# Kernel optimization log

Measured on AMD Instinct MI355X. Metric: run time of the kernel, lower is better.

The kernel has to match this reference:

```python
import jax, jax.numpy as jnp
import numpy as np

B, T, E, H = 2, 4096, 1024, 16
SEGS = (256, 512, 1024, 2048, 4096)
DILS = (1, 2, 4, 8, 16)
NEG = -1e8  # torchscale uses -1e8 for uncovered / masked lse entries


def setup_inputs() -> dict:
    key = jax.random.key(0)
    ks = jax.random.split(key, 5)
    sc = 0.02
    zb = jnp.zeros((E,), jnp.float32)
    return {
        "x": jax.random.normal(ks[0], (B, T, E), jnp.float32),
        "wq": jax.random.normal(ks[1], (E, E), jnp.float32) * sc,
        "bq": zb,
        "wk": jax.random.normal(ks[2], (E, E), jnp.float32) * sc,
        "bk": zb,
        "wv": jax.random.normal(ks[3], (E, E), jnp.float32) * sc,
        "bv": zb,
        "wo": jax.random.normal(ks[4], (E, E), jnp.float32) * sc,
        "bo": zb,
    }


def _scale_attn(q, k, v, w, r):
    # One LongNet scale: segment length w, dilation ratio r.
    # Head group g = head // (H//r) attends to in-segment positions p with p % r == g
    # (torchscale dense_to_sparse diagonal over (r1, r2)).
    Bq, Tq, Hq, d = q.shape
    n, s, hp = Tq // w, w // r, Hq // r  # segments, sparse length, heads per group

    def gather(x):
        # [B,T,H,d] -> segments [B,n,w,H,d]; split w=(s,r1) (p=l*r+r1) and H=(r2,hp);
        # keep diagonal r1 == r2.
        x = x.reshape(Bq, n, s, r, r, hp, d)
        x = jnp.diagonal(x, axis1=3, axis2=4)          # [B,n,s,hp,d,r]
        return jnp.moveaxis(x, -1, 3).reshape(Bq, n, s, Hq, d)

    qs, ks_, vs = gather(q), gather(k), gather(v)
    scores = jnp.einsum('bnqhd,bnkhd->bnhqk', qs, ks_)
    mask = jnp.tril(jnp.ones((s, s), dtype=bool))       # causal within sparse segment
    scores = jnp.where(mask, scores, NEG)
    lse = jax.scipy.special.logsumexp(scores, axis=-1)  # [B,n,h,q]
    out = jnp.einsum('bnhqk,bnkhd->bnqhd', jax.nn.softmax(scores, axis=-1), vs)

    # Scatter back to dense positions (sparse_to_dense): uncovered -> out 0, lse -1e8.
    eye = jnp.eye(r, dtype=out.dtype)
    out_g = out.reshape(Bq, n, s, r, hp, d)                               # heads as (g, hp)
    dense = jnp.einsum('bnsghd,pg->bnspghd', out_g, eye).reshape(Bq, Tq, Hq, d)
    lse_g = jnp.transpose(lse, (0, 1, 3, 2)).reshape(Bq, n, s, r, hp)     # [B,n,s,g,hp]
    lse_d = jnp.where(eye[:, :, None] > 0, lse_g[:, :, :, None, :, :], NEG)
    return dense, lse_d.reshape(Bq, Tq, Hq)


def reference(x, wq, bq, wk, bk, wv, bv, wo, bo):
    d = E // H
    q = (x @ wq + bq).reshape(B, T, H, d) * (d ** -0.5)
    k = (x @ wk + bk).reshape(B, T, H, d)
    v = (x @ wv + bv).reshape(B, T, H, d)
    outs, lses = [], []
    for w_, r_ in zip(SEGS, DILS):
        o, l = _scale_attn(q, k, v, w_, r_)
        outs.append(o)
        lses.append(l)
    # Merge scales with softmax over per-scale log-sum-exp (dense-attention equivalence).
    wgt = jax.nn.softmax(jnp.stack(lses), axis=0)[..., None]  # [S,B,T,H,1]
    y = jnp.sum(jnp.stack(outs) * wgt, axis=0).reshape(B, T, E)
    return y @ wo + bo
```

## Files before the change

### kernel.cpp

```cpp
#include <hip/hip_runtime.h>
#include <hip/hip_bf16.h>

typedef __bf16 bf16_t;
typedef __bf16 bf16x8 __attribute__((ext_vector_type(8)));
typedef __bf16 bf16x4 __attribute__((ext_vector_type(4)));
typedef float f32x4 __attribute__((ext_vector_type(4)));
typedef int vint4 __attribute__((ext_vector_type(4)));

#define AS1 __attribute__((address_space(1)))
#define AS3 __attribute__((address_space(3)))

constexpr int B_ = 2, T_ = 4096, E_ = 1024, H_ = 16;
constexpr int M_ = B_ * T_;

__device__ constexpr size_t OB_OFF[5]  = {0, 8388608, 12582912, 14680064, 15728640};
__device__ constexpr size_t LSE_OFF[5] = {0, 131072, 196608, 229376, 245760};
constexpr size_t OB_TOTAL  = 16252928;
constexpr size_t LSE_TOTAL = 253952;

__global__ __launch_bounds__(256) void cvt_f32_bf16(const float* __restrict__ in,
                                                    bf16_t* __restrict__ out) {
  int i = (blockIdx.x * 256 + threadIdx.x) * 4;
  const float4 v = *(const float4*)(in + i);
  bf16x4 o;
  o[0] = (bf16_t)v.x; o[1] = (bf16_t)v.y; o[2] = (bf16_t)v.z; o[3] = (bf16_t)v.w;
  *(bf16x4*)(out + i) = o;
}

__global__ __launch_bounds__(256) void cvt_transpose_w(
    const float* __restrict__ w0, const float* __restrict__ w1,
    const float* __restrict__ w2, const float* __restrict__ w3,
    bf16_t* __restrict__ o0, bf16_t* __restrict__ o1,
    bf16_t* __restrict__ o2, bf16_t* __restrict__ o3) {
  __shared__ float tile[32][33];
  const float* src; bf16_t* dst;
  switch (blockIdx.z) {
    case 0: src = w0; dst = o0; break;
    case 1: src = w1; dst = o1; break;
    case 2: src = w2; dst = o2; break;
    default: src = w3; dst = o3; break;
  }
  const int n0 = blockIdx.x * 32, k0 = blockIdx.y * 32;
  const int tx = threadIdx.x & 31, ty = threadIdx.x >> 5;
#pragma unroll
  for (int i = 0; i < 32; i += 8)
    tile[ty + i][tx] = src[(size_t)(k0 + ty + i) * E_ + n0 + tx];
  __syncthreads();
#pragma unroll
  for (int i = 0; i < 32; i += 8)
    dst[(size_t)(n0 + ty + i) * E_ + k0 + tx] = (bf16_t)tile[tx][ty + i];
}

template <bool OUT_BF16, bool QKV>
__global__ __launch_bounds__(512, 1) void gemm256(
    const bf16_t* __restrict__ A, const bf16_t* __restrict__ BT,
    const float* __restrict__ bias0, const float* __restrict__ bias1,
    const float* __restrict__ bias2, void* __restrict__ Cout) {
  constexpr int K = E_;
  constexpr int NT = K / 64;
  __shared__ bf16_t Sm[65536];

  const int tid = threadIdx.x;
  const int lane = tid & 63;
  const int wid = tid >> 6;
  const int wm = wid >> 2, wn = wid & 3;
  const int lc = lane & 15, lg = lane >> 4;
  const int bm = blockIdx.x;
  int bn = blockIdx.y;

  const float* bias = bias0;
  float scale = 1.0f;
  void* outp = Cout;
  const bf16_t* Bt = BT;
  if (QKV) {
    const int which = bn >> 2;
    bn &= 3;
    bias = (which == 0) ? bias0 : (which == 1) ? bias1 : bias2;
    scale = (which == 0) ? 0.125f : 1.0f;
    outp = (void*)((bf16_t*)Cout + (size_t)which * M_ * E_);
    Bt += (size_t)which * E_ * E_;
  }

  const int srow = tid >> 3;
  const int schunk = (tid & 7) ^ (srow & 7);
  const bf16_t* Ag = A + (size_t)(bm * 256 + srow) * K + schunk * 8;
  const bf16_t* Bg = Bt + (size_t)(bn * 256 + srow) * K + schunk * 8;

  auto stA = [&](int kt, int bu) {
#pragma unroll
    for (int l = 0; l < 4; ++l)
      __builtin_amdgcn_global_load_lds(
          (const AS1 void*)(Ag + (size_t)(l * 64) * K + kt * 64),
          (AS3 void*)(Sm + bu * 32768 + l * 4096 + tid * 8), 16, 0, 0);
  };
  auto stB = [&](int kt, int bu) {
#pragma unroll
    for (int l = 0; l < 4; ++l)
      __builtin_amdgcn_global_load_lds(
          (const AS1 void*)(Bg + (size_t)(l * 64) * K + kt * 64),
          (AS3 void*)(Sm + bu * 32768 + 16384 + l * 4096 + tid * 8), 16, 0, 0);
  };

  f32x4 acc[8][4] = {};

  stA(0, 0); stB(0, 0);
  stA(1, 1); stB(1, 1);
  asm volatile("s_waitcnt vmcnt(8)" ::: "memory");
  __builtin_amdgcn_s_barrier();
  asm volatile("" ::: "memory");

  for (int kt = 0; kt < NT; ++kt) {
    const int bc = kt & 1;
    const bf16_t* Sa = Sm + bc * 32768;
    const bf16_t* Sb = Sm + bc * 32768 + 16384;
    const bool st = (kt + 2) < NT;

#pragma unroll
    for (int kk = 0; kk < 2; ++kk) {
      bf16x8 afr[8], bfr[4];
      const int sl = ((kk * 4 + lg) ^ (lc & 7)) * 8;
#pragma unroll
      for (int i = 0; i < 8; ++i)
        afr[i] = *(const bf16x8*)&Sa[(wm * 128 + i * 16 + lc) * 64 + sl];
#pragma unroll
      for (int j = 0; j < 4; ++j)
        bfr[j] = *(const bf16x8*)&Sb[(wn * 64 + j * 16 + lc) * 64 + sl];
      if (kk == 1 && st) {
        asm volatile("s_waitcnt lgkmcnt(0)" ::: "memory");
        __builtin_amdgcn_s_barrier();
        stA(kt + 2, bc); stB(kt + 2, bc);
      }
      __builtin_amdgcn_s_setprio(1);
#pragma unroll
      for (int i = 0; i < 8; ++i)
#pragma unroll
        for (int j = 0; j < 4; ++j)
          acc[i][j] = __builtin_amdgcn_mfma_f32_16x16x32_bf16(afr[i], bfr[j], acc[i][j], 0, 0, 0);
      __builtin_amdgcn_s_setprio(0);
    }
    if (st)                asm volatile("s_waitcnt vmcnt(8)" ::: "memory");
    else if (kt + 1 < NT)  asm volatile("s_waitcnt vmcnt(0)" ::: "memory");
    if (kt + 1 < NT) {
      __builtin_amdgcn_s_barrier();
      asm volatile("" ::: "memory");
    }
  }

#pragma unroll
  for (int i = 0; i < 8; ++i) {
    const int row = bm * 256 + wm * 128 + i * 16 + lg * 4;
#pragma unroll
    for (int j = 0; j < 4; ++j) {
      const int col = bn * 256 + wn * 64 + j * 16 + lc;
      const float bv = bias[col];
#pragma unroll
      for (int rg = 0; rg < 4; ++rg) {
        const float v = (acc[i][j][rg] + bv) * scale;
        if (OUT_BF16)
          ((bf16_t*)outp)[(size_t)(row + rg) * E_ + col] = (bf16_t)v;
        else
          ((float*)outp)[(size_t)(row + rg) * E_ + col] = v;
      }
    }
  }
}

template <bool OUT_BF16, bool QKV>
__global__ __launch_bounds__(512, 1) void gemm_dp(
    const bf16_t* __restrict__ A, const bf16_t* __restrict__ BT,
    const float* __restrict__ bias0, const float* __restrict__ bias1,
    const float* __restrict__ bias2, void* __restrict__ Cout) {
  constexpr int K = E_;
  constexpr int NT = K / 64;
  __shared__ bf16_t Sm[73728];

  const int tid = threadIdx.x;
  const int lane = tid & 63;
  const int wid = tid >> 6;
  const int wm = wid >> 1, wn = wid & 1;
  const int lc = lane & 15, lg = lane >> 4;
  const int bm = blockIdx.x;
  int bn = blockIdx.y;

  const float* bias = bias0;
  float scale = 1.0f;
  void* outp = Cout;
  const bf16_t* Bt = BT;
  if (QKV) {
    const int which = bn >> 3;
    bn &= 7;
    bias = (which == 0) ? bias0 : (which == 1) ? bias1 : bias2;
    scale = (which == 0) ? 0.125f : 1.0f;
    outp = (void*)((bf16_t*)Cout + (size_t)which * M_ * E_);
    Bt += (size_t)which * E_ * E_;
  }

  const int srow = tid >> 3;
  const int schunk = (tid & 7) ^ (srow & 7);
  const bf16_t* Ag = A + (size_t)(bm * 256 + srow) * K + schunk * 8;
  const bf16_t* Bg = Bt + (size_t)(bn * 128 + srow) * K + schunk * 8;

  auto stA = [&](int kt, int bu) {
#pragma unroll
    for (int l = 0; l < 4; ++l)
      __builtin_amdgcn_global_load_lds(
          (const AS1 void*)(Ag + (size_t)(l * 64) * K + kt * 64),
          (AS3 void*)(Sm + bu * 16384 + l * 4096 + tid * 8), 16, 0, 0);
  };
  auto stB = [&](int kt, int bu) {
#pragma unroll
    for (int l = 0; l < 2; ++l)
      __builtin_amdgcn_global_load_lds(
          (const AS1 void*)(Bg + (size_t)(l * 64) * K + kt * 64),
          (AS3 void*)(Sm + 49152 + bu * 8192 + l * 4096 + tid * 8), 16, 0, 0);
  };

  const int sl0 = ((lg) ^ (lc & 7)) * 8;
  const int sl1 = ((4 + lg) ^ (lc & 7)) * 8;

  f32x4 acc[4][4] = {};

  stA(0, 0); stB(0, 0);
  stA(1, 1); stB(1, 1);

  for (int kt = 0; kt < NT; ++kt) {
    const int bc = kt % 3;
    if (kt + 2 < NT) {
      const int bs = (kt + 2) % 3;
      stA(kt + 2, bs); stB(kt + 2, bs);
      asm volatile("s_waitcnt vmcnt(12)" ::: "memory");
    } else if (kt + 1 < NT) {
      asm volatile("s_waitcnt vmcnt(6)" ::: "memory");
    } else {
      asm volatile("s_waitcnt vmcnt(0)" ::: "memory");
    }
    __builtin_amdgcn_s_barrier();
    asm volatile("" ::: "memory");

    const int ab = bc * 16384 + (wm * 64 + lc) * 64;
    const int bb = 49152 + bc * 8192 + (wn * 64 + lc) * 64;
    bf16x8 afr[4][2], bfr[4][2];
#pragma unroll
    for (int i = 0; i < 4; ++i) {
      afr[i][0] = *(const bf16x8*)&Sm[ab + i * 1024 + sl0];
      afr[i][1] = *(const bf16x8*)&Sm[ab + i * 1024 + sl1];
    }
#pragma unroll
    for (int j = 0; j < 4; ++j) {
      bfr[j][0] = *(const bf16x8*)&Sm[bb + j * 1024 + sl0];
      bfr[j][1] = *(const bf16x8*)&Sm[bb + j * 1024 + sl1];
    }
#pragma unroll
    for (int i = 0; i < 4; ++i)
#pragma unroll
      for (int j = 0; j < 4; ++j) {
        acc[i][j] = __builtin_amdgcn_mfma_f32_16x16x32_bf16(afr[i][0], bfr[j][0], acc[i][j], 0, 0, 0);
        acc[i][j] = __builtin_amdgcn_mfma_f32_16x16x32_bf16(afr[i][1], bfr[j][1], acc[i][j], 0, 0, 0);
      }
    asm volatile("" ::: "memory");
    __builtin_amdgcn_s_barrier();
  }

#pragma unroll
  for (int i = 0; i < 4; ++i) {
    const int row = bm * 256 + wm * 64 + i * 16 + lg * 4;
#pragma unroll
    for (int j = 0; j < 4; ++j) {
      const int col = bn * 128 + wn * 64 + j * 16 + lc;
      const float bv = bias[col];
#pragma unroll
      for (int rg = 0; rg < 4; ++rg) {
        const float v = (acc[i][j][rg] + bv) * scale;
        if (OUT_BF16)
          ((bf16_t*)outp)[(size_t)(row + rg) * E_ + col] = (bf16_t)v;
        else
          ((float*)outp)[(size_t)(row + rg) * E_ + col] = v;
      }
    }
  }
}

__global__ __launch_bounds__(512, 4) void attn_inst(
    const bf16_t* __restrict__ Q, const bf16_t* __restrict__ K,
    const bf16_t* __restrict__ V, bf16_t* __restrict__ Ob,
    float* __restrict__ Lse) {
  __shared__ alignas(16) bf16_t Ks[256][72];
  __shared__ alignas(16) bf16_t Vt[64][264];
  __shared__ alignas(16) bf16_t Pw[8][16][40];

  const int bid = blockIdx.x;
  int s, ibase;
  if (bid < 512)      { s = 0; ibase = 0; }
  else if (bid < 768) { s = 1; ibase = 512; }
  else if (bid < 896) { s = 2; ibase = 768; }
  else if (bid < 960) { s = 3; ibase = 896; }
  else                { s = 4; ibase = 960; }
  const int inst = bid - ibase;
  const int h = inst & 15;
  const int nseg_log = 4 - s;
  const int seg = (inst >> 4) & ((1 << nseg_log) - 1);
  const int b = inst >> (4 + nseg_log);
  const int g = h >> (4 - s);

  const int t = threadIdx.x;
  const int lane = t & 63;
  const int wv = t >> 6;
  const int lc = lane & 15;
  const int lg = lane >> 4;

  {
    const int row = t >> 1, ch = (t & 1) * 32;
    const int tk = ((seg * 256 + row) << s) + g;
    const size_t off = ((size_t)b * T_ + tk) * E_ + h * 64 + ch;
    const bf16_t* Kg = K + off;
    const bf16_t* Vg = V + off;
#pragma unroll
    for (int j = 0; j < 4; ++j)
      *(bf16x8*)&Ks[row][ch + j * 8] = *(const bf16x8*)(Kg + j * 8);
#pragma unroll
    for (int j = 0; j < 4; ++j) {
      bf16x8 va = *(const bf16x8*)(Vg + j * 8);
#pragma unroll
      for (int e = 0; e < 8; ++e) Vt[ch + j * 8 + e][row] = va[e];
    }
  }
  __syncthreads();

  const size_t rowbase = (size_t)(b * H_ + h) * (T_ >> s) + seg * 256;

#pragma unroll
  for (int sel = 0; sel < 2; ++sel) {
    const int tile = sel ? (15 - wv) : wv;
    const int q = tile * 16 + lc;

    const int tq = ((seg * 256 + q) << s) + g;
    const bf16_t* Qg = Q + ((size_t)b * T_ + tq) * E_ + h * 64 + lg * 8;
    bf16x8 qfrag0 = *(const bf16x8*)(Qg);
    bf16x8 qfrag1 = *(const bf16x8*)(Qg + 32);

    float m = -INFINITY, Z = 0.0f;
    f32x4 Oa[4] = {};

    const int nkb = tile / 2 + 1;
    const int diag = tile / 2;
    for (int kb = 0; kb < nkb; ++kb) {
      f32x4 sacc[2] = {};
      __builtin_amdgcn_s_setprio(1);
#pragma unroll
      for (int kt = 0; kt < 2; ++kt) {
        bf16x8 kf0 = *(const bf16x8*)&Ks[kb * 32 + kt * 16 + lc][lg * 8];
        bf16x8 kf1 = *(const bf16x8*)&Ks[kb * 32 + kt * 16 + lc][32 + lg * 8];
        sacc[kt] = __builtin_amdgcn_mfma_f32_16x16x32_bf16(kf0, qfrag0, sacc[kt], 0, 0, 0);
        sacc[kt] = __builtin_amdgcn_mfma_f32_16x16x32_bf16(kf1, qfrag1, sacc[kt], 0, 0, 0);
      }
      __builtin_amdgcn_s_setprio(0);
      if (kb == diag) {
#pragma unroll
        for (int kt = 0; kt < 2; ++kt)
#pragma unroll
          for (int rg = 0; rg < 4; ++rg)
            if (kb * 32 + kt * 16 + lg * 4 + rg > q) sacc[kt][rg] = -1e30f;
      }
      float pm = fmaxf(fmaxf(fmaxf(sacc[0][0], sacc[0][1]), fmaxf(sacc[0][2], sacc[0][3])),
                       fmaxf(fmaxf(sacc[1][0], sacc[1][1]), fmaxf(sacc[1][2], sacc[1][3])));
      pm = fmaxf(pm, __shfl_xor(pm, 16));
      pm = fmaxf(pm, __shfl_xor(pm, 32));
      const float nm = fmaxf(m, pm);
      const float crr = __expf(m - nm);
      m = nm;
      float psum = 0.0f;
#pragma unroll
      for (int kt = 0; kt < 2; ++kt)
#pragma unroll
        for (int rg = 0; rg < 4; ++rg) {
          const float p = __expf(sacc[kt][rg] - nm);
          psum += p;
          Pw[wv][lc][kt * 16 + lg * 4 + rg] = (bf16_t)p;
        }
      psum += __shfl_xor(psum, 16);
      psum += __shfl_xor(psum, 32);
      Z = Z * crr + psum;
#pragma unroll
      for (int dt = 0; dt < 4; ++dt)
#pragma unroll
        for (int rg = 0; rg < 4; ++rg) Oa[dt][rg] *= crr;
      bf16x8 pb = *(const bf16x8*)&Pw[wv][lc][lg * 8];
      __builtin_amdgcn_s_setprio(1);
#pragma unroll
      for (int dt = 0; dt < 4; ++dt) {
        bf16x8 vf = *(const bf16x8*)&Vt[dt * 16 + lc][kb * 32 + lg * 8];
        Oa[dt] = __builtin_amdgcn_mfma_f32_16x16x32_bf16(vf, pb, Oa[dt], 0, 0, 0);
      }
      __builtin_amdgcn_s_setprio(0);
    }

    const float lse = m + __logf(Z);
    const float iZ = 1.0f / Z;
    bf16_t* orow = Ob + OB_OFF[s] + (rowbase + q) * 64 + lg * 4;
#pragma unroll
    for (int dt = 0; dt < 4; ++dt) {
      bf16x4 ov;
      ov[0] = (bf16_t)(Oa[dt][0] * iZ);
      ov[1] = (bf16_t)(Oa[dt][1] * iZ);
      ov[2] = (bf16_t)(Oa[dt][2] * iZ);
      ov[3] = (bf16_t)(Oa[dt][3] * iZ);
      *(bf16x4*)(orow + dt * 16) = ov;
    }
    if (lg == 0) Lse[LSE_OFF[s] + rowbase + q] = lse;
  }
}

__global__ __launch_bounds__(256) void attn_merge(const bf16_t* __restrict__ Ob,
                                                  const float* __restrict__ Lse,
                                                  bf16_t* __restrict__ Y) {
  const int gtid = blockIdx.x * 256 + threadIdx.x;
  const int d8 = gtid & 7;
  const int h = (gtid >> 3) & 15;
  const int tt = (gtid >> 7) & (T_ - 1);
  const int b = gtid >> 19;

  float m = -INFINITY, S = 0.0f;
  float acc[8];
#pragma unroll
  for (int j = 0; j < 8; ++j) acc[j] = 0.0f;

#pragma unroll
  for (int s = 0; s < 5; ++s) {
    const int r = 1 << s;
    const int g = h >> (4 - s);
    if ((tt & (r - 1)) != g) continue;
    const size_t idx = (size_t)(b * H_ + h) * (T_ >> s) + (tt >> s);
    const float lse = Lse[LSE_OFF[s] + idx];
    const bf16x8 ov = *(const bf16x8*)(Ob + OB_OFF[s] + idx * 64 + d8 * 8);
    const float nM = fmaxf(m, lse);
    const float a = __expf(m - nM);
    const float e = __expf(lse - nM);
#pragma unroll
    for (int j = 0; j < 8; ++j) acc[j] = acc[j] * a + (float)ov[j] * e;
    S = S * a + e;
    m = nM;
  }

  const float invS = 1.0f / S;
  bf16x8 o;
#pragma unroll
  for (int j = 0; j < 8; ++j) o[j] = (bf16_t)(acc[j] * invS);
  *(bf16x8*)(Y + (size_t)gtid * 8) = o;
}

extern "C" void kernel_launch(void* const* d_in, const int* in_sizes, int n_in,
                              void* d_out, int out_size, void* d_ws, size_t ws_size,
                              hipStream_t stream) {
  (void)in_sizes; (void)n_in; (void)out_size; (void)ws_size;
  const float* x  = (const float*)d_in[0];
  const float* wq = (const float*)d_in[1];
  const float* bq = (const float*)d_in[2];
  const float* wk = (const float*)d_in[3];
  const float* bk = (const float*)d_in[4];
  const float* wv = (const float*)d_in[5];
  const float* bv = (const float*)d_in[6];
  const float* wo = (const float*)d_in[7];
  const float* bo = (const float*)d_in[8];

  char* p = (char*)d_ws;
  auto take = [&](size_t bytes) {
    char* q = p;
    p += (bytes + 255) & ~(size_t)255;
    return (void*)q;
  };
  bf16_t* wq_t = (bf16_t*)take((size_t)E_ * E_ * 2);
  bf16_t* wk_t = (bf16_t*)take((size_t)E_ * E_ * 2);
  bf16_t* wv_t = (bf16_t*)take((size_t)E_ * E_ * 2);
  bf16_t* wo_t = (bf16_t*)take((size_t)E_ * E_ * 2);
  bf16_t* xb   = (bf16_t*)take((size_t)M_ * E_ * 2);
  bf16_t* qb   = (bf16_t*)take((size_t)M_ * E_ * 2);
  bf16_t* kbuf = (bf16_t*)take((size_t)M_ * E_ * 2);
  bf16_t* vbuf = (bf16_t*)take((size_t)M_ * E_ * 2);
  bf16_t* yb   = (bf16_t*)take((size_t)M_ * E_ * 2);
  bf16_t* Ob   = (bf16_t*)take(OB_TOTAL * 2);
  float*  Lse  = (float*)take(LSE_TOTAL * 4);
  (void)wk_t; (void)wv_t;

  cvt_f32_bf16<<<M_ * E_ / 1024, 256, 0, stream>>>(x, xb);
  cvt_transpose_w<<<dim3(32, 32, 4), 256, 0, stream>>>(wq, wk, wv, wo, wq_t, wk_t, wv_t, wo_t);

  gemm256<true, true><<<dim3(M_ / 256, 12), 512, 0, stream>>>(
      xb, wq_t, bq, bk, bv, qb);

  attn_inst<<<992, 512, 0, stream>>>(qb, kbuf, vbuf, Ob, Lse);

  attn_merge<<<M_ * E_ / 8 / 256, 256, 0, stream>>>(Ob, Lse, yb);

  gemm_dp<false, false><<<dim3(M_ / 256, 8), 512, 0, stream>>>(
      yb, wo_t, bo, bo, bo, d_out);
}
```

Before: 139.7 us.

## Restructure QKV GEMM main loop into phased LDS reads interleaved with prefetches

The QKV projection GEMM's k-loop is split into four phases per tile. Each phase reads a slice of A fragments, issues part of the next tiles' global-to-LDS loads, and runs a smaller MFMA batch, with barriers between phases. The goal is to spread memory traffic across the loop and overlap it with MFMA work, instead of doing one bulk load and one big barrier per tile. This adds more barriers per iteration and relies on a tight vmcnt bookkeeping scheme, which risks stalls or hazards on the LDS buffers.

```diff
diff --git a/kernel.cpp b/kernel.cpp
--- a/kernel.cpp
+++ b/kernel.cpp
@@ -52,7 +52,7 @@
 }
 
 template <bool OUT_BF16, bool QKV>
-__global__ __launch_bounds__(512, 1) void gemm256(
+__global__ __launch_bounds__(512, 1) void gemm8ph(
     const bf16_t* __restrict__ A, const bf16_t* __restrict__ BT,
     const float* __restrict__ bias0, const float* __restrict__ bias1,
     const float* __restrict__ bias2, void* __restrict__ Cout) {
@@ -86,63 +86,76 @@
   const bf16_t* Ag = A + (size_t)(bm * 256 + srow) * K + schunk * 8;
   const bf16_t* Bg = Bt + (size_t)(bn * 256 + srow) * K + schunk * 8;
 
-  auto stA = [&](int kt, int bu) {
-#pragma unroll
-    for (int l = 0; l < 4; ++l)
-      __builtin_amdgcn_global_load_lds(
-          (const AS1 void*)(Ag + (size_t)(l * 64) * K + kt * 64),
-          (AS3 void*)(Sm + bu * 32768 + l * 4096 + tid * 8), 16, 0, 0);
+  auto ldA = [&](int kt, int l) {
+    __builtin_amdgcn_global_load_lds(
+        (const AS1 void*)(Ag + (size_t)(l * 64) * K + kt * 64),
+        (AS3 void*)(Sm + (kt & 1) * 32768 + l * 4096 + tid * 8), 16, 0, 0);
   };
-  auto stB = [&](int kt, int bu) {
-#pragma unroll
-    for (int l = 0; l < 4; ++l)
-      __builtin_amdgcn_global_load_lds(
-          (const AS1 void*)(Bg + (size_t)(l * 64) * K + kt * 64),
-          (AS3 void*)(Sm + bu * 32768 + 16384 + l * 4096 + tid * 8), 16, 0, 0);
+  auto ldB = [&](int kt, int l) {
+    __builtin_amdgcn_global_load_lds(
+        (const AS1 void*)(Bg + (size_t)(l * 64) * K + kt * 64),
+        (AS3 void*)(Sm + (kt & 1) * 32768 + 16384 + l * 4096 + tid * 8), 16, 0, 0);
   };
 
   f32x4 acc[8][4] = {};
 
-  stA(0, 0); stB(0, 0);
-  stA(1, 1); stB(1, 1);
-  asm volatile("s_waitcnt vmcnt(8)" ::: "memory");
+  ldA(0, 0); ldA(0, 1); ldA(0, 2); ldA(0, 3);
+  ldB(0, 0); ldB(0, 1); ldB(0, 2); ldB(0, 3);
+  ldB(1, 0); ldB(1, 1); ldB(1, 2); ldB(1, 3);
+  ldA(1, 0); ldA(1, 2);
+  asm volatile("s_waitcnt vmcnt(6)" ::: "memory");
   __builtin_amdgcn_s_barrier();
-  asm volatile("" ::: "memory");
-
+
+  const int sxor = (lc & 7);
   for (int kt = 0; kt < NT; ++kt) {
-    const int bc = kt & 1;
-    const bf16_t* Sa = Sm + bc * 32768;
-    const bf16_t* Sb = Sm + bc * 32768 + 16384;
-    const bool st = (kt + 2) < NT;
-
-#pragma unroll
-    for (int kk = 0; kk < 2; ++kk) {
-      bf16x8 afr[8], bfr[4];
-      const int sl = ((kk * 4 + lg) ^ (lc & 7)) * 8;
-#pragma unroll
-      for (int i = 0; i < 8; ++i)
-        afr[i] = *(const bf16x8*)&Sa[(wm * 128 + i * 16 + lc) * 64 + sl];
-#pragma unroll
-      for (int j = 0; j < 4; ++j)
-        bfr[j] = *(const bf16x8*)&Sb[(wn * 64 + j * 16 + lc) * 64 + sl];
-      if (kk == 1 && st) {
-        asm volatile("s_waitcnt lgkmcnt(0)" ::: "memory");
-        __builtin_amdgcn_s_barrier();
-        stA(kt + 2, bc); stB(kt + 2, bc);
-      }
+    const int sa = (kt & 1) * 32768;
+    const int sb = sa + 16384;
+    const bool st1 = (kt + 1) < NT;
+    const bool st2 = (kt + 2) < NT;
+    bf16x8 bfr[4][2];
+
+#pragma unroll
+    for (int p = 0; p < 4; ++p) {
+      asm volatile("" ::: "memory");
+      bf16x8 afr[2][2];
+#pragma unroll
+      for (int i2 = 0; i2 < 2; ++i2) {
+        const int row = wm * 128 + p * 32 + i2 * 16 + lc;
+        afr[i2][0] = *(const bf16x8*)&Sm[sa + row * 64 + ((0 * 4 + lg) ^ sxor) * 8];
+        afr[i2][1] = *(const bf16x8*)&Sm[sa + row * 64 + ((1 * 4 + lg) ^ sxor) * 8];
+      }
+      if (p == 0) {
+#pragma unroll
+        for (int j = 0; j < 4; ++j) {
+          const int row = wn * 64 + j * 16 + lc;
+          bfr[j][0] = *(const bf16x8*)&Sm[sb + row * 64 + ((0 * 4 + lg) ^ sxor) * 8];
+          bfr[j][1] = *(const bf16x8*)&Sm[sb + row * 64 + ((1 * 4 + lg) ^ sxor) * 8];
+        }
+      }
+      if (p == 0) { if (st1) ldA(kt + 1, 1); }
+      else if (p == 1) { if (st1) ldA(kt + 1, 3); }
+      else if (p == 2) { if (st2) { ldB(kt + 2, 0); ldB(kt + 2, 1); ldA(kt + 2, 0); } }
+      else             { if (st2) { ldB(kt + 2, 2); ldB(kt + 2, 3); ldA(kt + 2, 2); } }
+
+      __builtin_amdgcn_s_barrier();
+      asm volatile("s_waitcnt lgkmcnt(0)" ::: "memory");
       __builtin_amdgcn_s_setprio(1);
 #pragma unroll
-      for (int i = 0; i < 8; ++i)
-#pragma unroll
-        for (int j = 0; j < 4; ++j)
-          acc[i][j] = __builtin_amdgcn_mfma_f32_16x16x32_bf16(afr[i], bfr[j], acc[i][j], 0, 0, 0);
+      for (int i2 = 0; i2 < 2; ++i2)
+#pragma unroll
+        for (int j = 0; j < 4; ++j) {
+          acc[p * 2 + i2][j] = __builtin_amdgcn_mfma_f32_16x16x32_bf16(
+              afr[i2][0], bfr[j][0], acc[p * 2 + i2][j], 0, 0, 0);
+          acc[p * 2 + i2][j] = __builtin_amdgcn_mfma_f32_16x16x32_bf16(
+              afr[i2][1], bfr[j][1], acc[p * 2 + i2][j], 0, 0, 0);
+        }
       __builtin_amdgcn_s_setprio(0);
-    }
-    if (st)                asm volatile("s_waitcnt vmcnt(8)" ::: "memory");
-    else if (kt + 1 < NT)  asm volatile("s_waitcnt vmcnt(0)" ::: "memory");
-    if (kt + 1 < NT) {
+      if (p == 3) {
+        if (st2)      asm volatile("s_waitcnt vmcnt(6)" ::: "memory");
+        else if (st1) asm volatile("s_waitcnt vmcnt(0)" ::: "memory");
+      }
+      asm volatile("" ::: "memory");
       __builtin_amdgcn_s_barrier();
-      asm volatile("" ::: "memory");
     }
   }
 
@@ -484,7 +497,7 @@
   cvt_f32_bf16<<<M_ * E_ / 1024, 256, 0, stream>>>(x, xb);
   cvt_transpose_w<<<dim3(32, 32, 4), 256, 0, stream>>>(wq, wk, wv, wo, wq_t, wk_t, wv_t, wo_t);
 
-  gemm256<true, true><<<dim3(M_ / 256, 12), 512, 0, stream>>>(
+  gemm8ph<true, true><<<dim3(M_ / 256, 12), 512, 0, stream>>>(
       xb, wq_t, bq, bk, bv, qb);
 
   attn_inst<<<992, 512, 0, stream>>>(qb, kbuf, vbuf, Ob, Lse);
```

After: 145.1 us. 3.9% more time.
